# Performance work log

Hardware: AMD Instinct MI355X
Metric: run time of the kernel (lower is better)

Reference implementation:

```python
import jax, jax.numpy as jnp
import numpy as np

B, T, D_ENC, D_DEC, D_ATT = 64, 4096, 512, 512, 256


def setup_inputs() -> dict:
    keys = jax.random.split(jax.random.key(0), 8)
    h_enc = jax.random.normal(keys[0], (B, T, D_ENC), dtype=jnp.float32)
    h_dec = jax.random.normal(keys[1], (B, 1, D_DEC), dtype=jnp.float32)
    mask = jax.random.randint(keys[2], (B, T), 0, 2).astype(bool)
    s = 0.02
    Wq_w = jax.random.normal(keys[3], (D_ATT, D_DEC), dtype=jnp.float32) * s
    Wq_b = jnp.zeros((D_ATT,), dtype=jnp.float32)
    Wk_w = jax.random.normal(keys[4], (D_ATT, D_ENC), dtype=jnp.float32) * s
    Wk_b = jnp.zeros((D_ATT,), dtype=jnp.float32)
    v_w = jax.random.normal(keys[5], (1, D_ATT), dtype=jnp.float32) * s
    return {"h_enc": h_enc, "h_dec": h_dec, "Wq_w": Wq_w, "Wq_b": Wq_b,
            "Wk_w": Wk_w, "Wk_b": Wk_b, "v_w": v_w, "mask": mask}


def reference(h_enc, h_dec, Wq_w, Wq_b, Wk_w, Wk_b, v_w, mask):
    # q: [B,1,d_att], k: [B,T,d_att]
    q = jnp.einsum('bqe,ae->bqa', h_dec, Wq_w) + Wq_b
    k = jnp.einsum('bte,ae->bta', h_enc, Wk_w) + Wk_b
    # additive (Bahdanau) score: v^T tanh(q + k) -> [B,T]
    scores = jnp.einsum('bta,a->bt', jnp.tanh(q + k), v_w[0])
    scores = jnp.where(mask, scores, jnp.float32(-1e9))
    w = jax.nn.softmax(scores, axis=1)          # [B,T]
    ctx = jnp.einsum('bt,bte->be', w, h_enc)    # [B,d_enc]
    return ctx, w
```

## Files before the change

### kernel.cpp

```cpp
#include <hip/hip_runtime.h>
#include <math.h>

#define B    64
#define T    4096
#define DENC 512
#define DDEC 512
#define DATT 256

typedef __attribute__((ext_vector_type(8))) short  short8;
typedef __attribute__((ext_vector_type(4))) float  f32x4;

__device__ __forceinline__ unsigned short f2bf(float f) {
    union { float f; unsigned u; } v; v.f = f;
    return (unsigned short)((v.u + 0x7fffu + ((v.u >> 16) & 1u)) >> 16);
}

__device__ __forceinline__ float tanh_fast(float x) {
    float e = __expf(2.0f * x);
    return 1.0f - 2.0f / (e + 1.0f);
}

__global__ __launch_bounds__(256) void k_wkconv(const float* __restrict__ Wk_w,
                                                unsigned short* __restrict__ WkB) {
    int i = (blockIdx.x * 256 + threadIdx.x) * 4;
    float4 v = *(const float4*)(Wk_w + i);
    ushort4 o;
    o.x = f2bf(v.x); o.y = f2bf(v.y); o.z = f2bf(v.z); o.w = f2bf(v.w);
    *(ushort4*)(WkB + i) = o;
}

__global__ __launch_bounds__(256) void k_qproj(const float* __restrict__ h_dec,
                                               const float* __restrict__ Wq_w,
                                               const float* __restrict__ Wq_b,
                                               const float* __restrict__ Wk_b,
                                               float* __restrict__ qq) {
    __shared__ float sh[DDEC];
    const int b = blockIdx.x;
    const int tid = threadIdx.x;
    ((float2*)sh)[tid] = ((const float2*)(h_dec + (size_t)b * DDEC))[tid];
    __syncthreads();
    const int a = tid;
    const float4* wr  = (const float4*)(Wq_w + (size_t)a * DDEC);
    const float4* shv = (const float4*)sh;
    float acc = 0.f;
#pragma unroll 4
    for (int i = 0; i < DDEC / 4; ++i) {
        float4 wv = wr[i];
        float4 hv = shv[i];
        acc += wv.x * hv.x + wv.y * hv.y + wv.z * hv.z + wv.w * hv.w;
    }
    qq[b * DATT + a] = acc + Wq_b[a] + Wk_b[a];
}

#define BM 128
#define BK 32

__global__ __launch_bounds__(256, 2) void k_score(const float* __restrict__ h_enc,
                                                  const unsigned short* __restrict__ WkB,
                                                  const float* __restrict__ qq,
                                                  const float* __restrict__ v_w,
                                                  const int* __restrict__ mask,
                                                  float* __restrict__ scores) {
    __shared__ short As[BM * BK];
    __shared__ short Bs[DATT * BK];
    __shared__ float sp[2][BM];

    const int tc   = blockIdx.x;
    const int b    = blockIdx.y;
    const int tid  = threadIdx.x;
    const int wv   = tid >> 6;
    const int lane = tid & 63;
    const int ln15 = lane & 15;
    const int qd   = lane >> 4;
    const int wv_t = wv >> 1;
    const int wv_a = wv & 1;
    const int t0   = tc * BM;

    f32x4 acc[4][8];
#pragma unroll
    for (int i = 0; i < 4; ++i)
#pragma unroll
        for (int j = 0; j < 8; ++j) acc[i][j] = (f32x4){0.f, 0.f, 0.f, 0.f};

    const float* Abase = h_enc + ((size_t)b * T + t0) * DENC;

    for (int k0 = 0; k0 < DENC; k0 += BK) {
#pragma unroll
        for (int it = 0; it < 4; ++it) {
            int idx = (wv * 4 + it) * 64 + lane;
            int r   = idx >> 2;
            int cc  = (idx & 3) ^ ((r >> 1) & 3);
            const unsigned short* gp = WkB + (size_t)r * DENC + k0 + cc * 8;
            short* lp = &Bs[(wv * 4 + it) * 64 * 8];
            __builtin_amdgcn_global_load_lds(
                (const __attribute__((address_space(1))) unsigned int*)gp,
                (__attribute__((address_space(3))) unsigned int*)lp, 16, 0, 0);
        }
#pragma unroll
        for (int it = 0; it < 2; ++it) {
            int idx = it * 256 + tid;
            int r   = idx >> 2;
            int cc  = (idx & 3) ^ ((r >> 1) & 3);
            const float* gp = Abase + (size_t)r * DENC + k0 + cc * 8;
            float4 v0 = *(const float4*)gp;
            float4 v1 = *(const float4*)(gp + 4);
            short8 pk;
            pk[0] = (short)f2bf(v0.x); pk[1] = (short)f2bf(v0.y);
            pk[2] = (short)f2bf(v0.z); pk[3] = (short)f2bf(v0.w);
            pk[4] = (short)f2bf(v1.x); pk[5] = (short)f2bf(v1.y);
            pk[6] = (short)f2bf(v1.z); pk[7] = (short)f2bf(v1.w);
            *(short8*)&As[idx * 8] = pk;
        }
        __syncthreads();

        short8 af[4], bfr[8];
#pragma unroll
        for (int ti = 0; ti < 4; ++ti) {
            int r = wv_t * 64 + ti * 16 + ln15;
            int s = qd ^ ((r >> 1) & 3);
            af[ti] = *(const short8*)&As[r * 32 + s * 8];
        }
#pragma unroll
        for (int tj = 0; tj < 8; ++tj) {
            int r = wv_a * 128 + tj * 16 + ln15;
            int s = qd ^ ((r >> 1) & 3);
            bfr[tj] = *(const short8*)&Bs[r * 32 + s * 8];
        }
#pragma unroll
        for (int ti = 0; ti < 4; ++ti)
#pragma unroll
            for (int tj = 0; tj < 8; ++tj)
                acc[ti][tj] = __builtin_amdgcn_mfma_f32_16x16x32_bf16(
                    af[ti], bfr[tj], acc[ti][tj], 0, 0, 0);
        __syncthreads();
    }

    float qr[8], vr[8];
#pragma unroll
    for (int tj = 0; tj < 8; ++tj) {
        int a = wv_a * 128 + tj * 16 + ln15;
        qr[tj] = qq[b * DATT + a];
        vr[tj] = v_w[a];
    }
#pragma unroll
    for (int ti = 0; ti < 4; ++ti) {
#pragma unroll
        for (int rg = 0; rg < 4; ++rg) {
            float s = 0.f;
#pragma unroll
            for (int tj = 0; tj < 8; ++tj)
                s += vr[tj] * tanh_fast(qr[tj] + acc[ti][tj][rg]);
            s += __shfl_xor(s, 1, 64);
            s += __shfl_xor(s, 2, 64);
            s += __shfl_xor(s, 4, 64);
            s += __shfl_xor(s, 8, 64);
            if (ln15 == 0)
                sp[wv_a][wv_t * 64 + ti * 16 + qd * 4 + rg] = s;
        }
    }
    __syncthreads();
    if (tid < BM) {
        int t = t0 + tid;
        float s = sp[0][tid] + sp[1][tid];
        bool m = mask[(size_t)b * T + t] != 0;
        scores[(size_t)b * T + t] = m ? s : -1e9f;
    }
}

__global__ __launch_bounds__(256) void k_softmax(float* __restrict__ w) {
    const int b = blockIdx.x;
    const int tid = threadIdx.x;
    const int wid = tid >> 6, lane = tid & 63;
    float* row = w + (size_t)b * T;
    __shared__ float red[4];
    __shared__ float bmax_s, bsum_s;

    float x[T / 256];
#pragma unroll
    for (int i = 0; i < T / 256; ++i) x[i] = row[tid + i * 256];

    float lmax = -INFINITY;
#pragma unroll
    for (int i = 0; i < T / 256; ++i) lmax = fmaxf(lmax, x[i]);
#pragma unroll
    for (int off = 32; off >= 1; off >>= 1) lmax = fmaxf(lmax, __shfl_xor(lmax, off, 64));
    if (lane == 0) red[wid] = lmax;
    __syncthreads();
    if (tid == 0) bmax_s = fmaxf(fmaxf(red[0], red[1]), fmaxf(red[2], red[3]));
    __syncthreads();
    const float bmax = bmax_s;

    float lsum = 0.f;
#pragma unroll
    for (int i = 0; i < T / 256; ++i) { x[i] = __expf(x[i] - bmax); lsum += x[i]; }
#pragma unroll
    for (int off = 32; off >= 1; off >>= 1) lsum += __shfl_xor(lsum, off, 64);
    if (lane == 0) red[wid] = lsum;
    __syncthreads();
    if (tid == 0) bsum_s = red[0] + red[1] + red[2] + red[3];
    __syncthreads();
    const float inv = 1.f / bsum_s;
#pragma unroll
    for (int i = 0; i < T / 256; ++i) row[tid + i * 256] = x[i] * inv;
}

#define TCH 256
__global__ __launch_bounds__(256) void k_ctx(const float* __restrict__ h_enc,
                                             const float* __restrict__ w,
                                             float* __restrict__ ctx) {
    const int b   = blockIdx.y;
    const int t0  = blockIdx.x * TCH;
    const int tid = threadIdx.x;
    __shared__ float ws[TCH];
    __shared__ float red[128][4];
    ws[tid] = w[(size_t)b * T + t0 + tid];
    __syncthreads();
    const int e4 = tid & 127, tp = tid >> 7;
    const float4* hb = (const float4*)(h_enc + ((size_t)b * T + t0) * DENC);
    float ax = 0.f, ay = 0.f, az = 0.f, aw = 0.f;
#pragma unroll 4
    for (int t = tp; t < TCH; t += 2) {
        float wt = ws[t];
        float4 hv = hb[(size_t)t * 128 + e4];
        ax = fmaf(wt, hv.x, ax);
        ay = fmaf(wt, hv.y, ay);
        az = fmaf(wt, hv.z, az);
        aw = fmaf(wt, hv.w, aw);
    }
    if (tp) { red[e4][0] = ax; red[e4][1] = ay; red[e4][2] = az; red[e4][3] = aw; }
    __syncthreads();
    if (!tp) {
        ax += red[e4][0]; ay += red[e4][1]; az += red[e4][2]; aw += red[e4][3];
        float* c = ctx + b * DENC + e4 * 4;
        atomicAdd(c + 0, ax);
        atomicAdd(c + 1, ay);
        atomicAdd(c + 2, az);
        atomicAdd(c + 3, aw);
    }
}

extern "C" void kernel_launch(void* const* d_in, const int* in_sizes, int n_in,
                              void* d_out, int out_size, void* d_ws, size_t ws_size,
                              hipStream_t stream) {
    const float* h_enc = (const float*)d_in[0];
    const float* h_dec = (const float*)d_in[1];
    const float* Wq_w  = (const float*)d_in[2];
    const float* Wq_b  = (const float*)d_in[3];
    const float* Wk_w  = (const float*)d_in[4];
    const float* Wk_b  = (const float*)d_in[5];
    const float* v_w   = (const float*)d_in[6];
    const int*   mask  = (const int*)d_in[7];

    float* out = (float*)d_out;
    float* ctx = out;
    float* wts = out + B * DENC;
    float*          qq  = (float*)d_ws;
    unsigned short* WkB = (unsigned short*)((char*)d_ws + B * DATT * 4);

    hipMemsetAsync(ctx, 0, (size_t)B * DENC * sizeof(float), stream);

    k_wkconv<<<DATT * DENC / 4 / 256, 256, 0, stream>>>(Wk_w, WkB);
    k_qproj<<<B, 256, 0, stream>>>(h_dec, Wq_w, Wq_b, Wk_b, qq);
    k_score<<<dim3(T / BM, B), 256, 0, stream>>>(h_enc, WkB, qq, v_w, mask, wts);
    k_softmax<<<B, 256, 0, stream>>>(wts);
    k_ctx<<<dim3(T / TCH, B), 256, 0, stream>>>(h_enc, wts, ctx);
}
```

Before: 837.4 us.

## Write bf16 copy of h_enc in score kernel and reuse it for context pass

The score GEMM kernel now stores its bf16-converted h_enc tile to a workspace buffer. The context reduction reads that half-size copy instead of re-reading fp32 h_enc, with wider 8-element loads and a larger time chunk. The float-to-bf16 packing uses a cheaper perm-based round-half-up. This trades an extra global write for a smaller second read and lowers ctx precision to bf16.

```diff
diff --git a/kernel.cpp b/kernel.cpp
--- a/kernel.cpp
+++ b/kernel.cpp
@@ -7,12 +7,23 @@
 #define DDEC 512
 #define DATT 256
 
-typedef __attribute__((ext_vector_type(8))) short  short8;
-typedef __attribute__((ext_vector_type(4))) float  f32x4;
+typedef __attribute__((ext_vector_type(8))) short          short8;
+typedef __attribute__((ext_vector_type(8))) unsigned short ushort8v;
+typedef __attribute__((ext_vector_type(4))) float          f32x4;
 
 __device__ __forceinline__ unsigned short f2bf(float f) {
     union { float f; unsigned u; } v; v.f = f;
     return (unsigned short)((v.u + 0x7fffu + ((v.u >> 16) & 1u)) >> 16);
+}
+
+__device__ __forceinline__ unsigned pk2bf(float a, float b) {
+    unsigned ua = __float_as_uint(a) + 0x8000u;
+    unsigned ub = __float_as_uint(b) + 0x8000u;
+    return __builtin_amdgcn_perm(ub, ua, 0x07060302u);
+}
+
+__device__ __forceinline__ float bf2f(unsigned short u) {
+    return __uint_as_float((unsigned)u << 16);
 }
 
 __device__ __forceinline__ float tanh_fast(float x) {
@@ -60,6 +71,7 @@
                                                   const float* __restrict__ qq,
                                                   const float* __restrict__ v_w,
                                                   const int* __restrict__ mask,
+                                                  unsigned short* __restrict__ hB,
                                                   float* __restrict__ scores) {
     __shared__ short As[BM * BK];
     __shared__ short Bs[DATT * BK];
@@ -83,6 +95,7 @@
         for (int j = 0; j < 8; ++j) acc[i][j] = (f32x4){0.f, 0.f, 0.f, 0.f};
 
     const float* Abase = h_enc + ((size_t)b * T + t0) * DENC;
+    unsigned short* hBbase = hB + ((size_t)b * T + t0) * DENC;
 
     for (int k0 = 0; k0 < DENC; k0 += BK) {
 #pragma unroll
@@ -104,12 +117,13 @@
             const float* gp = Abase + (size_t)r * DENC + k0 + cc * 8;
             float4 v0 = *(const float4*)gp;
             float4 v1 = *(const float4*)(gp + 4);
-            short8 pk;
-            pk[0] = (short)f2bf(v0.x); pk[1] = (short)f2bf(v0.y);
-            pk[2] = (short)f2bf(v0.z); pk[3] = (short)f2bf(v0.w);
-            pk[4] = (short)f2bf(v1.x); pk[5] = (short)f2bf(v1.y);
-            pk[6] = (short)f2bf(v1.z); pk[7] = (short)f2bf(v1.w);
-            *(short8*)&As[idx * 8] = pk;
+            uint4 pk;
+            pk.x = pk2bf(v0.x, v0.y);
+            pk.y = pk2bf(v0.z, v0.w);
+            pk.z = pk2bf(v1.x, v1.y);
+            pk.w = pk2bf(v1.z, v1.w);
+            *(uint4*)&As[idx * 8] = pk;
+            *(uint4*)(hBbase + (size_t)r * DENC + k0 + cc * 8) = pk;
         }
         __syncthreads();
 
@@ -204,38 +218,47 @@
     for (int i = 0; i < T / 256; ++i) row[tid + i * 256] = x[i] * inv;
 }
 
-#define TCH 256
-__global__ __launch_bounds__(256) void k_ctx(const float* __restrict__ h_enc,
+#define TCH 512
+__global__ __launch_bounds__(256) void k_ctx(const unsigned short* __restrict__ hB,
                                              const float* __restrict__ w,
                                              float* __restrict__ ctx) {
     const int b   = blockIdx.y;
     const int t0  = blockIdx.x * TCH;
     const int tid = threadIdx.x;
+    const int lane = tid & 63, wv = tid >> 6;
+    const int e8 = lane * 8;
     __shared__ float ws[TCH];
-    __shared__ float red[128][4];
-    ws[tid] = w[(size_t)b * T + t0 + tid];
-    __syncthreads();
-    const int e4 = tid & 127, tp = tid >> 7;
-    const float4* hb = (const float4*)(h_enc + ((size_t)b * T + t0) * DENC);
-    float ax = 0.f, ay = 0.f, az = 0.f, aw = 0.f;
+    __shared__ float red[3][DENC];
+
+    ((float2*)ws)[tid] = ((const float2*)(w + (size_t)b * T + t0))[tid];
+    __syncthreads();
+
+    const unsigned short* hp = hB + ((size_t)(b * T + t0 + wv)) * DENC + e8;
+    float a[8];
+#pragma unroll
+    for (int j = 0; j < 8; ++j) a[j] = 0.f;
+
 #pragma unroll 4
-    for (int t = tp; t < TCH; t += 2) {
+    for (int t = wv; t < TCH; t += 4) {
         float wt = ws[t];
-        float4 hv = hb[(size_t)t * 128 + e4];
-        ax = fmaf(wt, hv.x, ax);
-        ay = fmaf(wt, hv.y, ay);
-        az = fmaf(wt, hv.z, az);
-        aw = fmaf(wt, hv.w, aw);
-    }
-    if (tp) { red[e4][0] = ax; red[e4][1] = ay; red[e4][2] = az; red[e4][3] = aw; }
-    __syncthreads();
-    if (!tp) {
-        ax += red[e4][0]; ay += red[e4][1]; az += red[e4][2]; aw += red[e4][3];
-        float* c = ctx + b * DENC + e4 * 4;
-        atomicAdd(c + 0, ax);
-        atomicAdd(c + 1, ay);
-        atomicAdd(c + 2, az);
-        atomicAdd(c + 3, aw);
+        ushort8v hv = *(const ushort8v*)hp;
+        hp += (size_t)4 * DENC;
+#pragma unroll
+        for (int j = 0; j < 8; ++j)
+            a[j] = fmaf(wt, bf2f((unsigned short)hv[j]), a[j]);
+    }
+
+    if (wv > 0) {
+#pragma unroll
+        for (int j = 0; j < 8; ++j) red[wv - 1][e8 + j] = a[j];
+    }
+    __syncthreads();
+    if (wv == 0) {
+#pragma unroll
+        for (int j = 0; j < 8; ++j) {
+            float s = a[j] + red[0][e8 + j] + red[1][e8 + j] + red[2][e8 + j];
+            atomicAdd(&ctx[b * DENC + e8 + j], s);
+        }
     }
 }
 
@@ -254,14 +277,16 @@
     float* out = (float*)d_out;
     float* ctx = out;
     float* wts = out + B * DENC;
+
     float*          qq  = (float*)d_ws;
-    unsigned short* WkB = (unsigned short*)((char*)d_ws + B * DATT * 4);
+    unsigned short* WkB = (unsigned short*)((char*)d_ws + (64 << 10));
+    unsigned short* hB  = (unsigned short*)((char*)d_ws + (1 << 20));
 
     hipMemsetAsync(ctx, 0, (size_t)B * DENC * sizeof(float), stream);
 
     k_wkconv<<<DATT * DENC / 4 / 256, 256, 0, stream>>>(Wk_w, WkB);
     k_qproj<<<B, 256, 0, stream>>>(h_dec, Wq_w, Wq_b, Wk_b, qq);
-    k_score<<<dim3(T / BM, B), 256, 0, stream>>>(h_enc, WkB, qq, v_w, mask, wts);
+    k_score<<<dim3(T / BM, B), 256, 0, stream>>>(h_enc, WkB, qq, v_w, mask, hB, wts);
     k_softmax<<<B, 256, 0, stream>>>(wts);
-    k_ctx<<<dim3(T / TCH, B), 256, 0, stream>>>(h_enc, wts, ctx);
-}
+    k_ctx<<<dim3(T / TCH, B), 256, 0, stream>>>(hB, wts, ctx);
+}
```

After: 856.3 us. 2.3% more time.
